# Kernel optimization log

Measured on AMD Instinct MI355X. Metric: run time of the kernel, lower is better.

The kernel has to match this reference:

```python
import jax, jax.numpy as jnp
import numpy as np

IN_C = 128
KEY_C = 128
VAL_C = 128
HEADS = 8
N_CLS = 4

def setup_inputs() -> dict:
    key = jax.random.key(0)
    ks = jax.random.split(key, 10)
    n, c, d, h, w = 2, IN_C, 16, 64, 64
    x = jax.random.normal(ks[0], (n, c, d, h, w), dtype=jnp.float32)
    CLS = jax.random.normal(ks[1], (n, KEY_C, N_CLS), dtype=jnp.float32)
    s = 0.02
    Wk = jax.random.normal(ks[2], (KEY_C, IN_C), dtype=jnp.float32) * s
    bk = jnp.zeros((KEY_C,), dtype=jnp.float32)
    Wq = jax.random.normal(ks[3], (KEY_C, IN_C), dtype=jnp.float32) * s
    bq = jnp.zeros((KEY_C,), dtype=jnp.float32)
    Wv = jax.random.normal(ks[4], (VAL_C, IN_C), dtype=jnp.float32) * s
    bv = jnp.zeros((VAL_C,), dtype=jnp.float32)
    Wr = jax.random.normal(ks[5], (IN_C, VAL_C), dtype=jnp.float32) * s
    br = jnp.zeros((IN_C,), dtype=jnp.float32)
    return {"x": x, "CLS": CLS, "Wk": Wk, "bk": bk, "Wq": Wq, "bq": bq,
            "Wv": Wv, "bv": bv, "Wr": Wr, "br": br}

def reference(x, CLS, Wk, bk, Wq, bq, Wv, bv, Wr, br):
    n, c, d, h, w = x.shape
    L = d * h * w
    xf = x.reshape(n, c, L)
    # 1x1 Conv3d == channel matmul
    keys = jnp.einsum('oc,ncl->nol', Wk, xf) + bk[None, :, None]
    queries = jnp.einsum('oc,ncl->nol', Wq, xf) + bq[None, :, None]
    values = jnp.einsum('oc,ncl->nol', Wv, xf) + bv[None, :, None]
    # prepend CLS tokens along the sequence axis
    keys = jnp.concatenate([CLS, keys], axis=-1)      # (n, kc, L+4)
    queries = jnp.concatenate([CLS, queries], axis=-1)
    values = jnp.concatenate([CLS, values], axis=-1)
    Lt = L + N_CLS
    hk = KEY_C // HEADS
    hv = VAL_C // HEADS
    # contiguous channel slices per head == reshape (n, HEADS, hk, Lt)
    k = jax.nn.softmax(keys.reshape(n, HEADS, hk, Lt), axis=3)    # softmax over sequence
    q = jax.nn.softmax(queries.reshape(n, HEADS, hk, Lt), axis=2) # softmax over head channels
    v = values.reshape(n, HEADS, hv, Lt)
    context = jnp.einsum('nhkl,nhvl->nhkv', k, v)                 # (n, H, hk, hv)
    att = jnp.einsum('nhkv,nhkl->nhvl', context, q)               # (n, H, hv, Lt)
    # original loop reassigns CLS each head; final value comes from last head
    CLS_out = att[:, -1, :, :N_CLS]                               # (n, hv, 4)
    agg = att[:, :, :, N_CLS:].reshape(n, HEADS * hv, L)          # concat over heads
    attention = (jnp.einsum('oc,ncl->nol', Wr, agg) + br[None, :, None]).reshape(n, c, d, h, w)
    context_last = context[:, -1]                                 # last head's context
    return (attention, context_last, CLS_out)
```

## Files before the change

### kernel.cpp

```cpp
#include <hip/hip_runtime.h>

typedef unsigned short u16;
typedef short bf16x8 __attribute__((ext_vector_type(8)));
typedef short short4v __attribute__((ext_vector_type(4)));
typedef float floatx4 __attribute__((ext_vector_type(4)));

#define OUT_CTX 16777216
#define OUT_CLS (OUT_CTX + 512)

__device__ __forceinline__ u16 f2b(float f) {
  unsigned int u = __float_as_uint(f);
  u += 0x7fffu + ((u >> 16) & 1u);
  return (u16)(u >> 16);
}
__device__ __forceinline__ float b2f(u16 b) { return __uint_as_float(((unsigned int)b) << 16); }

__device__ __forceinline__ bf16x8 pack8(const float* p) {
  float4 a = *(const float4*)p;
  float4 b = *(const float4*)(p + 4);
  bf16x8 r;
  r[0] = (short)f2b(a.x); r[1] = (short)f2b(a.y); r[2] = (short)f2b(a.z); r[3] = (short)f2b(a.w);
  r[4] = (short)f2b(b.x); r[5] = (short)f2b(b.y); r[6] = (short)f2b(b.z); r[7] = (short)f2b(b.w);
  return r;
}

__device__ __forceinline__ float dot4(float4 a, float4 b) {
  return a.x * b.x + a.y * b.y + a.z * b.z + a.w * b.w;
}

__global__ __launch_bounds__(256) void kA(
    const float* __restrict__ x, const float* __restrict__ Wk,
    const float* __restrict__ bk, const float* __restrict__ Wv,
    const float* __restrict__ bv, float* __restrict__ S2,
    float* __restrict__ Cnum2) {
  __shared__ __align__(16) u16 xT[64][136];
  __shared__ __align__(16) u16 ev[256][72];
  const int t = threadIdx.x;
  const int w = t >> 6, lane = t & 63;
  const int quad = lane >> 4, lm = lane & 15;
  const int bid = blockIdx.x;
  const int n = bid >> 8;
  const int l0base = (bid & 255) << 8;
  const int slot = bid & 3;
  const int sc = t >> 4, sl4 = t & 15;

  float4 pf[8];
  #pragma unroll
  for (int i = 0; i < 8; ++i)
    pf[i] = *(const float4*)(x + (((size_t)(n * 128 + sc * 8 + i)) << 16) + l0base + sl4 * 4);

  bf16x8 wf[4][4];
  #pragma unroll
  for (int nt = 0; nt < 4; ++nt) {
    const float* W = (nt < 2) ? Wk : Wv;
    int row = w * 32 + (nt & 1) * 16 + lm;
    #pragma unroll
    for (int ks = 0; ks < 4; ++ks)
      wf[nt][ks] = pack8(W + row * 128 + ks * 32 + quad * 8);
  }
  float biasE[2] = { bk[w * 32 + lm], bk[w * 32 + 16 + lm] };
  float biasV[2] = { bv[w * 32 + lm], bv[w * 32 + 16 + lm] };

  floatx4 z4 = {0.f, 0.f, 0.f, 0.f};
  floatx4 cacc[2] = {z4, z4};
  float sacc[2] = {0.f, 0.f};

  for (int tile = 0; tile < 4; ++tile) {
    const float* pff = (const float*)pf;
    #pragma unroll
    for (int r = 0; r < 4; ++r) {
      bf16x8 vx;
      #pragma unroll
      for (int i = 0; i < 8; ++i) vx[i] = (short)f2b(pff[i * 4 + r]);
      *(bf16x8*)&xT[sl4 * 4 + r][sc * 8] = vx;
    }
    if (tile < 3) {
      int l0n = l0base + (tile + 1) * 64;
      #pragma unroll
      for (int i = 0; i < 8; ++i)
        pf[i] = *(const float4*)(x + (((size_t)(n * 128 + sc * 8 + i)) << 16) + l0n + sl4 * 4);
    }
    __syncthreads();

    floatx4 acc[4][4];
    #pragma unroll
    for (int mt = 0; mt < 4; ++mt)
      #pragma unroll
      for (int nt = 0; nt < 4; ++nt) acc[mt][nt] = z4;

    #pragma unroll
    for (int mt = 0; mt < 4; ++mt)
      #pragma unroll
      for (int ks = 0; ks < 4; ++ks) {
        bf16x8 xa = *(const bf16x8*)&xT[mt * 16 + lm][ks * 32 + quad * 8];
        #pragma unroll
        for (int nt = 0; nt < 4; ++nt)
          acc[mt][nt] = __builtin_amdgcn_mfma_f32_16x16x32_bf16(xa, wf[nt][ks], acc[mt][nt], 0, 0, 0);
      }
    __syncthreads();

    #pragma unroll
    for (int nt = 0; nt < 2; ++nt)
      #pragma unroll
      for (int mt = 0; mt < 4; ++mt) {
        short4v p;
        #pragma unroll
        for (int j = 0; j < 4; ++j) {
          float v = __expf(acc[mt][nt][j] + biasE[nt]);
          u16 b = f2b(v);
          sacc[nt] += b2f(b);
          p[j] = (short)b;
        }
        *(short4v*)&ev[w * 32 + nt * 16 + lm][mt * 16 + quad * 4] = p;
      }
    #pragma unroll
    for (int nt = 0; nt < 2; ++nt)
      #pragma unroll
      for (int mt = 0; mt < 4; ++mt) {
        short4v p;
        #pragma unroll
        for (int j = 0; j < 4; ++j)
          p[j] = (short)f2b(acc[mt][nt + 2][j] + biasV[nt]);
        *(short4v*)&ev[128 + w * 32 + nt * 16 + lm][mt * 16 + quad * 4] = p;
      }

    #pragma unroll
    for (int hh = 0; hh < 2; ++hh) {
      int h = w * 2 + hh;
      #pragma unroll
      for (int ks = 0; ks < 2; ++ks) {
        bf16x8 aE = *(const bf16x8*)&ev[h * 16 + lm][ks * 32 + quad * 8];
        bf16x8 bV = *(const bf16x8*)&ev[128 + h * 16 + lm][ks * 32 + quad * 8];
        cacc[hh] = __builtin_amdgcn_mfma_f32_16x16x32_bf16(aE, bV, cacc[hh], 0, 0, 0);
      }
    }
  }

  float* Cn = Cnum2 + slot * 4096;
  #pragma unroll
  for (int hh = 0; hh < 2; ++hh) {
    int h = w * 2 + hh;
    #pragma unroll
    for (int j = 0; j < 4; ++j)
      atomicAdd(&Cn[((n * 8 + h) * 16 + quad * 4 + j) * 16 + lm], cacc[hh][j]);
  }
  #pragma unroll
  for (int nt = 0; nt < 2; ++nt) {
    float s = sacc[nt];
    s += __shfl_xor(s, 16);
    s += __shfl_xor(s, 32);
    if (quad == 0)
      atomicAdd(&S2[slot * 256 + n * 128 + w * 32 + nt * 16 + lm], s);
  }
}

__global__ __launch_bounds__(256) void kB(
    const float* __restrict__ x, const float* __restrict__ CLS,
    const float* __restrict__ Wq, const float* __restrict__ bq,
    const float* __restrict__ Wr, const float* __restrict__ br,
    const float* __restrict__ S2, const float* __restrict__ Cnum2,
    float* __restrict__ out) {
  __shared__ __align__(16) u16 xT[64][136];
  __shared__ __align__(16) u16 ubuf[64 * 136];
  const int t = threadIdx.x;
  const int w = t >> 6, lane = t & 63;
  const int quad = lane >> 4, lm = lane & 15;
  const int bid = blockIdx.x;
  const int n = bid >> 9;
  const int l0base = (bid & 511) << 7;
  const int sc = t >> 4, sl4 = t & 15;

  float4 pf[8];
  #pragma unroll
  for (int i = 0; i < 8; ++i)
    pf[i] = *(const float4*)(x + (((size_t)(n * 128 + sc * 8 + i)) << 16) + l0base + sl4 * 4);

  bf16x8 wq[2][4];
  #pragma unroll
  for (int mt = 0; mt < 2; ++mt) {
    int row = (w * 2 + mt) * 16 + lm;
    #pragma unroll
    for (int ks = 0; ks < 4; ++ks)
      wq[mt][ks] = pack8(Wq + row * 128 + ks * 32 + quad * 8);
  }
  float bqv[2][4], brv[2][4];
  #pragma unroll
  for (int mt = 0; mt < 2; ++mt)
    #pragma unroll
    for (int j = 0; j < 4; ++j) {
      bqv[mt][j] = bq[(w * 2 + mt) * 16 + quad * 4 + j];
      brv[mt][j] = br[(w * 2 + mt) * 16 + quad * 4 + j];
    }

  float* ctxn = (float*)ubuf;
  {
    int hk = t >> 1, v0 = (t & 1) * 8;
    int hbase = hk & 0x70;
    float ek[4];
    float den = 0.f;
    #pragma unroll
    for (int j = 0; j < 4; ++j) {
      ek[j] = __expf(CLS[(n * 128 + hk) * 4 + j]);
      den += ek[j];
    }
    #pragma unroll
    for (int s = 0; s < 4; ++s) den += S2[s * 256 + n * 128 + hk];
    float inv = 1.f / den;
    float vv[8];
    #pragma unroll
    for (int i = 0; i < 8; ++i) {
      int v = v0 + i;
      float num = 0.f;
      #pragma unroll
      for (int s = 0; s < 4; ++s) num += Cnum2[s * 4096 + (n * 128 + hk) * 16 + v];
      #pragma unroll
      for (int j = 0; j < 4; ++j) num += ek[j] * CLS[(n * 128 + hbase + v) * 4 + j];
      vv[i] = num * inv;
    }
    float4 a = {vv[0], vv[1], vv[2], vv[3]}, b = {vv[4], vv[5], vv[6], vv[7]};
    *(float4*)&ctxn[hk * 16 + v0] = a;
    *(float4*)&ctxn[hk * 16 + v0 + 4] = b;
  }
  __syncthreads();

  if ((bid & 511) == 0) {
    {
      int kc = t >> 4, vc = t & 15;
      out[OUT_CTX + n * 256 + t] = ctxn[(112 + kc) * 16 + vc];
    }
    if (t < 64) {
      int vc = t >> 2, j = t & 3;
      float den = 0.f, num = 0.f;
      #pragma unroll
      for (int kc = 0; kc < 16; ++kc) {
        float e_ = __expf(CLS[(n * 128 + 112 + kc) * 4 + j]);
        den += e_;
        num += e_ * ctxn[(112 + kc) * 16 + vc];
      }
      out[OUT_CLS + n * 64 + t] = num / den;
    }
  }

  bf16x8 mA[2][4];
  for (int ks = 0; ks < 4; ++ks) {
    int h = 2 * ks + (quad >> 1);
    float4 wrv[2][4];
    #pragma unroll
    for (int mt = 0; mt < 2; ++mt) {
      const float* wp = Wr + ((w * 2 + mt) * 16 + lm) * 128 + h * 16;
      #pragma unroll
      for (int q4 = 0; q4 < 4; ++q4) wrv[mt][q4] = *(const float4*)(wp + q4 * 4);
    }
    short mr0[8], mr1[8];
    #pragma unroll
    for (int jj = 0; jj < 8; ++jj) {
      int k = (quad & 1) * 8 + jj;
      const float4* cp = (const float4*)&ctxn[(h * 16 + k) * 16];
      float4 c0 = cp[0], c1 = cp[1], c2 = cp[2], c3 = cp[3];
      float m0 = dot4(wrv[0][0], c0) + dot4(wrv[0][1], c1) + dot4(wrv[0][2], c2) + dot4(wrv[0][3], c3);
      float m1 = dot4(wrv[1][0], c0) + dot4(wrv[1][1], c1) + dot4(wrv[1][2], c2) + dot4(wrv[1][3], c3);
      mr0[jj] = (short)f2b(m0);
      mr1[jj] = (short)f2b(m1);
    }
    mA[0][ks] = *(bf16x8*)mr0;
    mA[1][ks] = *(bf16x8*)mr1;
  }

  u16 (*qT)[136] = (u16 (*)[136])ubuf;
  floatx4 z4 = {0.f, 0.f, 0.f, 0.f};
  for (int tile = 0; tile < 2; ++tile) {
    int l0 = l0base + tile * 64;
    const float* pff = (const float*)pf;
    #pragma unroll
    for (int r = 0; r < 4; ++r) {
      bf16x8 vx;
      #pragma unroll
      for (int i = 0; i < 8; ++i) vx[i] = (short)f2b(pff[i * 4 + r]);
      *(bf16x8*)&xT[sl4 * 4 + r][sc * 8] = vx;
    }
    if (tile < 1) {
      #pragma unroll
      for (int i = 0; i < 8; ++i)
        pf[i] = *(const float4*)(x + (((size_t)(n * 128 + sc * 8 + i)) << 16) + l0base + 64 + sl4 * 4);
    }
    __syncthreads();

    floatx4 acc[2][4];
    #pragma unroll
    for (int mt = 0; mt < 2; ++mt)
      #pragma unroll
      for (int nt = 0; nt < 4; ++nt) acc[mt][nt] = z4;

    #pragma unroll
    for (int nt = 0; nt < 4; ++nt)
      #pragma unroll
      for (int ks = 0; ks < 4; ++ks) {
        bf16x8 b = *(const bf16x8*)&xT[nt * 16 + lm][ks * 32 + quad * 8];
        #pragma unroll
        for (int mt = 0; mt < 2; ++mt)
          acc[mt][nt] = __builtin_amdgcn_mfma_f32_16x16x32_bf16(wq[mt][ks], b, acc[mt][nt], 0, 0, 0);
      }

    #pragma unroll
    for (int mt = 0; mt < 2; ++mt) {
      int h = w * 2 + mt;
      #pragma unroll
      for (int nt = 0; nt < 4; ++nt) {
        float e[4];
        float ssum = 0.f;
        #pragma unroll
        for (int j = 0; j < 4; ++j) {
          e[j] = __expf(acc[mt][nt][j] + bqv[mt][j]);
          ssum += e[j];
        }
        ssum += __shfl_xor(ssum, 16);
        ssum += __shfl_xor(ssum, 32);
        float inv = 1.f / ssum;
        short4v p;
        #pragma unroll
        for (int j = 0; j < 4; ++j) p[j] = (short)f2b(e[j] * inv);
        *(short4v*)&qT[nt * 16 + lm][h * 16 + quad * 4] = p;
      }
    }
    __syncthreads();

    floatx4 acc2[2][4];
    #pragma unroll
    for (int mt = 0; mt < 2; ++mt)
      #pragma unroll
      for (int nt = 0; nt < 4; ++nt) acc2[mt][nt] = z4;

    #pragma unroll
    for (int nt = 0; nt < 4; ++nt)
      #pragma unroll
      for (int ks = 0; ks < 4; ++ks) {
        bf16x8 b = *(const bf16x8*)&qT[nt * 16 + lm][ks * 32 + quad * 8];
        #pragma unroll
        for (int mt = 0; mt < 2; ++mt)
          acc2[mt][nt] = __builtin_amdgcn_mfma_f32_16x16x32_bf16(mA[mt][ks], b, acc2[mt][nt], 0, 0, 0);
      }

    #pragma unroll
    for (int mt = 0; mt < 2; ++mt)
      #pragma unroll
      for (int j = 0; j < 4; ++j) {
        int R = (w * 2 + mt) * 16 + quad * 4 + j;
        #pragma unroll
        for (int nt = 0; nt < 4; ++nt)
          out[(((size_t)(n * 128 + R)) << 16) + l0 + nt * 16 + lm] = acc2[mt][nt][j] + brv[mt][j];
      }
  }
}

extern "C" void kernel_launch(void* const* d_in, const int* in_sizes, int n_in,
                              void* d_out, int out_size, void* d_ws, size_t ws_size,
                              hipStream_t stream) {
  const float* x   = (const float*)d_in[0];
  const float* CLS = (const float*)d_in[1];
  const float* Wk  = (const float*)d_in[2];
  const float* bk  = (const float*)d_in[3];
  const float* Wq  = (const float*)d_in[4];
  const float* bq  = (const float*)d_in[5];
  const float* Wv  = (const float*)d_in[6];
  const float* bv  = (const float*)d_in[7];
  const float* Wr  = (const float*)d_in[8];
  const float* br  = (const float*)d_in[9];
  float* out = (float*)d_out;
  char* ws = (char*)d_ws;
  float* S2    = (float*)(ws + 0);
  float* Cnum2 = (float*)(ws + 4096);

  hipMemsetAsync(ws, 0, 69632, stream);
  kA<<<512, 256, 0, stream>>>(x, Wk, bk, Wv, bv, S2, Cnum2);
  kB<<<1024, 256, 0, stream>>>(x, CLS, Wq, bq, Wr, br, S2, Cnum2, out);
}
```

Measured before the change: 196.6 us.

## Compute context and Wr·context fragments once in last kA block; enlarge kB tiles

The last-finishing kA block, found through an atomic done counter, now finalises the normalised context, writes the context and CLS outputs, and precomputes the Wr·context bf16 MFMA fragments into workspace. Previously every kB block redid this per-block work. kB now just loads the prebuilt fragments and processes four 64-column tiles per block across 512 blocks, which halves the grid. The cost is a serial tail: a single block does the fragment computation at the end of kA, and kB has less parallelism.

```diff
diff --git a/kernel.cpp b/kernel.cpp
--- a/kernel.cpp
+++ b/kernel.cpp
@@ -7,6 +7,7 @@
 
 #define OUT_CTX 16777216
 #define OUT_CLS (OUT_CTX + 512)
+#define NBLK 512
 
 __device__ __forceinline__ u16 f2b(float f) {
   unsigned int u = __float_as_uint(f);
@@ -24,17 +25,20 @@
   return r;
 }
 
-__device__ __forceinline__ float dot4(float4 a, float4 b) {
-  return a.x * b.x + a.y * b.y + a.z * b.z + a.w * b.w;
+__device__ __forceinline__ float aql(const float* p) {
+  return __hip_atomic_load(p, __ATOMIC_ACQUIRE, __HIP_MEMORY_SCOPE_AGENT);
 }
 
 __global__ __launch_bounds__(256) void kA(
-    const float* __restrict__ x, const float* __restrict__ Wk,
-    const float* __restrict__ bk, const float* __restrict__ Wv,
-    const float* __restrict__ bv, float* __restrict__ S2,
-    float* __restrict__ Cnum2) {
+    const float* __restrict__ x, const float* __restrict__ CLS,
+    const float* __restrict__ Wk, const float* __restrict__ bk,
+    const float* __restrict__ Wv, const float* __restrict__ bv,
+    const float* __restrict__ Wr, float* __restrict__ S2,
+    float* __restrict__ Cnum2, unsigned int* __restrict__ done,
+    u16* __restrict__ mfrag, float* __restrict__ out) {
   __shared__ __align__(16) u16 xT[64][136];
   __shared__ __align__(16) u16 ev[256][72];
+  __shared__ unsigned int lastflag;
   const int t = threadIdx.x;
   const int w = t >> 6, lane = t & 63;
   const int quad = lane >> 4, lm = lane & 15;
@@ -152,22 +156,89 @@
     if (quad == 0)
       atomicAdd(&S2[slot * 256 + n * 128 + w * 32 + nt * 16 + lm], s);
   }
+
+  __syncthreads();
+  if (t == 0) {
+    __threadfence();
+    unsigned int old = __hip_atomic_fetch_add(done, 1u, __ATOMIC_ACQ_REL, __HIP_MEMORY_SCOPE_AGENT);
+    lastflag = (old == NBLK - 1) ? 1u : 0u;
+  }
+  __syncthreads();
+  if (!lastflag) return;
+
+  float* ctxn = (float*)ev;
+  {
+    float ek[4];
+    float den = 0.f;
+    #pragma unroll
+    for (int j = 0; j < 4; ++j) {
+      ek[j] = __expf(CLS[t * 4 + j]);
+      den += ek[j];
+    }
+    #pragma unroll
+    for (int s = 0; s < 4; ++s) den += aql(&S2[s * 256 + t]);
+    float inv = 1.f / den;
+    int nn = t >> 7;
+    int hbase = (t & 127) & 0x70;
+    #pragma unroll
+    for (int v = 0; v < 16; ++v) {
+      float num = 0.f;
+      #pragma unroll
+      for (int s = 0; s < 4; ++s) num += aql(&Cnum2[s * 4096 + t * 16 + v]);
+      #pragma unroll
+      for (int j = 0; j < 4; ++j) num += ek[j] * CLS[(nn * 128 + hbase + v) * 4 + j];
+      ctxn[t * 16 + v] = num * inv;
+    }
+  }
+  __syncthreads();
+
+  #pragma unroll
+  for (int e = t; e < 512; e += 256)
+    out[OUT_CTX + e] = ctxn[(((e >> 8) * 128 + 112 + ((e >> 4) & 15)) << 4) + (e & 15)];
+  if (t < 128) {
+    int nn = t >> 6, vc = (t >> 2) & 15, j = t & 3;
+    float den = 0.f, num = 0.f;
+    #pragma unroll
+    for (int kc = 0; kc < 16; ++kc) {
+      float e_ = __expf(CLS[(nn * 128 + 112 + kc) * 4 + j]);
+      den += e_;
+      num += e_ * ctxn[((nn * 128 + 112 + kc) << 4) + vc];
+    }
+    out[OUT_CLS + t] = num / den;
+  }
+
+  for (int i = 0; i < 128; ++i) {
+    int e = i * 256 + t;
+    int nn = e >> 14;
+    int rem = e & 16383;
+    int rb = rem >> 11;
+    int ks = (rem >> 9) & 3;
+    int ln = (rem >> 3) & 63;
+    int j = rem & 7;
+    int o = rb * 16 + (ln & 15);
+    int cc = ks * 32 + (ln >> 4) * 8 + j;
+    int h = cc >> 4, k = cc & 15;
+    const float* wp = Wr + o * 128 + h * 16;
+    const float* cp = ctxn + ((nn * 128 + h * 16 + k) << 4);
+    float m = 0.f;
+    #pragma unroll
+    for (int v = 0; v < 16; ++v) m += wp[v] * cp[v];
+    mfrag[e] = f2b(m);
+  }
 }
 
 __global__ __launch_bounds__(256) void kB(
-    const float* __restrict__ x, const float* __restrict__ CLS,
-    const float* __restrict__ Wq, const float* __restrict__ bq,
-    const float* __restrict__ Wr, const float* __restrict__ br,
-    const float* __restrict__ S2, const float* __restrict__ Cnum2,
-    float* __restrict__ out) {
+    const float* __restrict__ x, const float* __restrict__ Wq,
+    const float* __restrict__ bq, const float* __restrict__ br,
+    const u16* __restrict__ mfrag, float* __restrict__ out) {
   __shared__ __align__(16) u16 xT[64][136];
-  __shared__ __align__(16) u16 ubuf[64 * 136];
+  __shared__ __align__(16) u16 qT[64][136];
   const int t = threadIdx.x;
   const int w = t >> 6, lane = t & 63;
   const int quad = lane >> 4, lm = lane & 15;
   const int bid = blockIdx.x;
-  const int n = bid >> 9;
-  const int l0base = (bid & 511) << 7;
+  const int n = bid >> 8;
+  const int l0base = (bid & 255) << 8;
   const int sc = t >> 4, sl4 = t & 15;
 
   float4 pf[8];
@@ -175,13 +246,15 @@
   for (int i = 0; i < 8; ++i)
     pf[i] = *(const float4*)(x + (((size_t)(n * 128 + sc * 8 + i)) << 16) + l0base + sl4 * 4);
 
-  bf16x8 wq[2][4];
+  bf16x8 wq[2][4], mA[2][4];
   #pragma unroll
   for (int mt = 0; mt < 2; ++mt) {
     int row = (w * 2 + mt) * 16 + lm;
     #pragma unroll
-    for (int ks = 0; ks < 4; ++ks)
+    for (int ks = 0; ks < 4; ++ks) {
       wq[mt][ks] = pack8(Wq + row * 128 + ks * 32 + quad * 8);
+      mA[mt][ks] = *(const bf16x8*)(mfrag + ((((n * 8 + w * 2 + mt) * 4 + ks) * 64 + lane) * 8));
+    }
   }
   float bqv[2][4], brv[2][4];
   #pragma unroll
@@ -192,83 +265,8 @@
       brv[mt][j] = br[(w * 2 + mt) * 16 + quad * 4 + j];
     }
 
-  float* ctxn = (float*)ubuf;
-  {
-    int hk = t >> 1, v0 = (t & 1) * 8;
-    int hbase = hk & 0x70;
-    float ek[4];
-    float den = 0.f;
-    #pragma unroll
-    for (int j = 0; j < 4; ++j) {
-      ek[j] = __expf(CLS[(n * 128 + hk) * 4 + j]);
-      den += ek[j];
-    }
-    #pragma unroll
-    for (int s = 0; s < 4; ++s) den += S2[s * 256 + n * 128 + hk];
-    float inv = 1.f / den;
-    float vv[8];
-    #pragma unroll
-    for (int i = 0; i < 8; ++i) {
-      int v = v0 + i;
-      float num = 0.f;
-      #pragma unroll
-      for (int s = 0; s < 4; ++s) num += Cnum2[s * 4096 + (n * 128 + hk) * 16 + v];
-      #pragma unroll
-      for (int j = 0; j < 4; ++j) num += ek[j] * CLS[(n * 128 + hbase + v) * 4 + j];
-      vv[i] = num * inv;
-    }
-    float4 a = {vv[0], vv[1], vv[2], vv[3]}, b = {vv[4], vv[5], vv[6], vv[7]};
-    *(float4*)&ctxn[hk * 16 + v0] = a;
-    *(float4*)&ctxn[hk * 16 + v0 + 4] = b;
-  }
-  __syncthreads();
-
-  if ((bid & 511) == 0) {
-    {
-      int kc = t >> 4, vc = t & 15;
-      out[OUT_CTX + n * 256 + t] = ctxn[(112 + kc) * 16 + vc];
-    }
-    if (t < 64) {
-      int vc = t >> 2, j = t & 3;
-      float den = 0.f, num = 0.f;
-      #pragma unroll
-      for (int kc = 0; kc < 16; ++kc) {
-        float e_ = __expf(CLS[(n * 128 + 112 + kc) * 4 + j]);
-        den += e_;
-        num += e_ * ctxn[(112 + kc) * 16 + vc];
-      }
-      out[OUT_CLS + n * 64 + t] = num / den;
-    }
-  }
-
-  bf16x8 mA[2][4];
-  for (int ks = 0; ks < 4; ++ks) {
-    int h = 2 * ks + (quad >> 1);
-    float4 wrv[2][4];
-    #pragma unroll
-    for (int mt = 0; mt < 2; ++mt) {
-      const float* wp = Wr + ((w * 2 + mt) * 16 + lm) * 128 + h * 16;
-      #pragma unroll
-      for (int q4 = 0; q4 < 4; ++q4) wrv[mt][q4] = *(const float4*)(wp + q4 * 4);
-    }
-    short mr0[8], mr1[8];
-    #pragma unroll
-    for (int jj = 0; jj < 8; ++jj) {
-      int k = (quad & 1) * 8 + jj;
-      const float4* cp = (const float4*)&ctxn[(h * 16 + k) * 16];
-      float4 c0 = cp[0], c1 = cp[1], c2 = cp[2], c3 = cp[3];
-      float m0 = dot4(wrv[0][0], c0) + dot4(wrv[0][1], c1) + dot4(wrv[0][2], c2) + dot4(wrv[0][3], c3);
-      float m1 = dot4(wrv[1][0], c0) + dot4(wrv[1][1], c1) + dot4(wrv[1][2], c2) + dot4(wrv[1][3], c3);
-      mr0[jj] = (short)f2b(m0);
-      mr1[jj] = (short)f2b(m1);
-    }
-    mA[0][ks] = *(bf16x8*)mr0;
-    mA[1][ks] = *(bf16x8*)mr1;
-  }
-
-  u16 (*qT)[136] = (u16 (*)[136])ubuf;
   floatx4 z4 = {0.f, 0.f, 0.f, 0.f};
-  for (int tile = 0; tile < 2; ++tile) {
+  for (int tile = 0; tile < 4; ++tile) {
     int l0 = l0base + tile * 64;
     const float* pff = (const float*)pf;
     #pragma unroll
@@ -278,10 +276,11 @@
       for (int i = 0; i < 8; ++i) vx[i] = (short)f2b(pff[i * 4 + r]);
       *(bf16x8*)&xT[sl4 * 4 + r][sc * 8] = vx;
     }
-    if (tile < 1) {
+    if (tile < 3) {
+      int l0n = l0base + (tile + 1) * 64;
       #pragma unroll
       for (int i = 0; i < 8; ++i)
-        pf[i] = *(const float4*)(x + (((size_t)(n * 128 + sc * 8 + i)) << 16) + l0base + 64 + sl4 * 4);
+        pf[i] = *(const float4*)(x + (((size_t)(n * 128 + sc * 8 + i)) << 16) + l0n + sl4 * 4);
     }
     __syncthreads();
 
@@ -367,10 +366,12 @@
   const float* br  = (const float*)d_in[9];
   float* out = (float*)d_out;
   char* ws = (char*)d_ws;
-  float* S2    = (float*)(ws + 0);
-  float* Cnum2 = (float*)(ws + 4096);
-
-  hipMemsetAsync(ws, 0, 69632, stream);
-  kA<<<512, 256, 0, stream>>>(x, Wk, bk, Wv, bv, S2, Cnum2);
-  kB<<<1024, 256, 0, stream>>>(x, CLS, Wq, bq, Wr, br, S2, Cnum2, out);
-}
+  float* S2          = (float*)(ws + 0);
+  float* Cnum2       = (float*)(ws + 4096);
+  unsigned int* done = (unsigned int*)(ws + 69632);
+  u16* mfrag         = (u16*)(ws + 69696);
+
+  hipMemsetAsync(ws, 0, 69696, stream);
+  kA<<<NBLK, 256, 0, stream>>>(x, CLS, Wk, bk, Wv, bv, Wr, S2, Cnum2, done, mfrag, out);
+  kB<<<512, 256, 0, stream>>>(x, Wq, bq, br, mfrag, out);
+}
```

Result: slower. 238.3 us (+21.2%).

## Cache bf16 transposed x from first kernel and reuse it in second

Applied to the files above, without the earlier changes.

The first pass now writes the bf16-converted, position-major copy of x to workspace, so the second kernel reads half the bytes and skips the fp32-to-bf16 conversion and transpose. The second kernel also moves from 1024 blocks of 128 positions to 512 blocks of 256 positions, looping over four tiles. This spends an extra 32 MB write in the first kernel to save a 64 MB fp32 reread, and the larger blocks amortise the per-block weight and context setup. It relies on the workspace being large enough to hold the bf16 copy.

```diff
diff --git a/kernel.cpp b/kernel.cpp
--- a/kernel.cpp
+++ b/kernel.cpp
@@ -32,7 +32,7 @@
     const float* __restrict__ x, const float* __restrict__ Wk,
     const float* __restrict__ bk, const float* __restrict__ Wv,
     const float* __restrict__ bv, float* __restrict__ S2,
-    float* __restrict__ Cnum2) {
+    float* __restrict__ Cnum2, u16* __restrict__ xbf) {
   __shared__ __align__(16) u16 xT[64][136];
   __shared__ __align__(16) u16 ev[256][72];
   const int t = threadIdx.x;
@@ -66,6 +66,7 @@
   float sacc[2] = {0.f, 0.f};
 
   for (int tile = 0; tile < 4; ++tile) {
+    int l0 = l0base + tile * 64;
     const float* pff = (const float*)pf;
     #pragma unroll
     for (int r = 0; r < 4; ++r) {
@@ -73,6 +74,7 @@
       #pragma unroll
       for (int i = 0; i < 8; ++i) vx[i] = (short)f2b(pff[i * 4 + r]);
       *(bf16x8*)&xT[sl4 * 4 + r][sc * 8] = vx;
+      *(bf16x8*)(xbf + ((((size_t)n << 16) + l0 + sl4 * 4 + r) << 7) + sc * 8) = vx;
     }
     if (tile < 3) {
       int l0n = l0base + (tile + 1) * 64;
@@ -155,7 +157,7 @@
 }
 
 __global__ __launch_bounds__(256) void kB(
-    const float* __restrict__ x, const float* __restrict__ CLS,
+    const u16* __restrict__ xbf, const float* __restrict__ CLS,
     const float* __restrict__ Wq, const float* __restrict__ bq,
     const float* __restrict__ Wr, const float* __restrict__ br,
     const float* __restrict__ S2, const float* __restrict__ Cnum2,
@@ -166,14 +168,15 @@
   const int w = t >> 6, lane = t & 63;
   const int quad = lane >> 4, lm = lane & 15;
   const int bid = blockIdx.x;
-  const int n = bid >> 9;
-  const int l0base = (bid & 511) << 7;
-  const int sc = t >> 4, sl4 = t & 15;
-
-  float4 pf[8];
-  #pragma unroll
-  for (int i = 0; i < 8; ++i)
-    pf[i] = *(const float4*)(x + (((size_t)(n * 128 + sc * 8 + i)) << 16) + l0base + sl4 * 4);
+  const int n = bid >> 8;
+  const int l0base = (bid & 255) << 8;
+  const int sl = t >> 2;
+  const int scq = t & 3;
+
+  bf16x8 pfb[4];
+  #pragma unroll
+  for (int k = 0; k < 4; ++k)
+    pfb[k] = *(const bf16x8*)(xbf + ((((size_t)n << 16) + l0base + sl) << 7) + scq * 32 + k * 8);
 
   bf16x8 wq[2][4];
   #pragma unroll
@@ -223,7 +226,7 @@
   }
   __syncthreads();
 
-  if ((bid & 511) == 0) {
+  if ((bid & 255) == 0) {
     {
       int kc = t >> 4, vc = t & 15;
       out[OUT_CTX + n * 256 + t] = ctxn[(112 + kc) * 16 + vc];
@@ -268,20 +271,16 @@
 
   u16 (*qT)[136] = (u16 (*)[136])ubuf;
   floatx4 z4 = {0.f, 0.f, 0.f, 0.f};
-  for (int tile = 0; tile < 2; ++tile) {
+  for (int tile = 0; tile < 4; ++tile) {
     int l0 = l0base + tile * 64;
-    const float* pff = (const float*)pf;
-    #pragma unroll
-    for (int r = 0; r < 4; ++r) {
-      bf16x8 vx;
-      #pragma unroll
-      for (int i = 0; i < 8; ++i) vx[i] = (short)f2b(pff[i * 4 + r]);
-      *(bf16x8*)&xT[sl4 * 4 + r][sc * 8] = vx;
-    }
-    if (tile < 1) {
-      #pragma unroll
-      for (int i = 0; i < 8; ++i)
-        pf[i] = *(const float4*)(x + (((size_t)(n * 128 + sc * 8 + i)) << 16) + l0base + 64 + sl4 * 4);
+    #pragma unroll
+    for (int k = 0; k < 4; ++k)
+      *(bf16x8*)&xT[sl][scq * 32 + k * 8] = pfb[k];
+    if (tile < 3) {
+      int l0n = l0base + (tile + 1) * 64;
+      #pragma unroll
+      for (int k = 0; k < 4; ++k)
+        pfb[k] = *(const bf16x8*)(xbf + ((((size_t)n << 16) + l0n + sl) << 7) + scq * 32 + k * 8);
     }
     __syncthreads();
 
@@ -369,8 +368,9 @@
   char* ws = (char*)d_ws;
   float* S2    = (float*)(ws + 0);
   float* Cnum2 = (float*)(ws + 4096);
+  u16* xbf     = (u16*)(ws + 69632);
 
   hipMemsetAsync(ws, 0, 69632, stream);
-  kA<<<512, 256, 0, stream>>>(x, Wk, bk, Wv, bv, S2, Cnum2);
-  kB<<<1024, 256, 0, stream>>>(x, CLS, Wq, bq, Wr, br, S2, Cnum2, out);
-}
+  kA<<<512, 256, 0, stream>>>(x, Wk, bk, Wv, bv, S2, Cnum2, xbf);
+  kB<<<512, 256, 0, stream>>>(xbf, CLS, Wq, bq, Wr, br, S2, Cnum2, out);
+}
```

Result: faster. 179.1 us (-8.9%).
